# Kernel tuning notes

Hardware: AMD Instinct MI355X
Metric: run time of the kernel (lower is better)

## Reference

```python
import jax, jax.numpy as jnp
import numpy as np

B, CL, H, W, NP = 128, 8, 16, 16, 32   # batch, primary cap length, height, width, n primary capsules
NC, CLO, ITER = 10, 16, 3              # n output capsules, output capsule length, routing iterations


def squash(t):
    # TensorMONK Activations 'squash': squash along axis 2 of a 3D tensor
    ss = jnp.sum(t * t, axis=2, keepdims=True)
    return (ss / (1.0 + ss)) * t / jnp.sqrt(ss)


def setup_inputs() -> dict:
    key = jax.random.key(0)
    k1, k2 = jax.random.split(key)
    tensor = jax.random.normal(k1, (B, CL, H, W, NP), dtype=jnp.float32)
    # nn.Parameter(torch.randn(...).normal_(0.0, 0.1)) -> N(0, 0.1)
    weight = 0.1 * jax.random.normal(k2, (CL * H * W, NP, NC * CLO), dtype=jnp.float32)
    return {"tensor": tensor, "weight": weight}


def reference(tensor, weight):
    b, cl, h, w, n_prim = tensor.shape
    # flatten spatial/length dims, squash along primary-capsule axis (dim 2, faithful to source)
    x = squash(tensor.reshape(b, -1, n_prim))                  # (B, P, N) with P = cl*h*w
    # (B,P,1,N) @ (P,N,K) broadcasted matmul -> (B,P,K)
    u = jnp.einsum('bpn,pnk->bpk', x, weight)
    u = u.reshape(b, cl, h, w, NC, CLO)                        # (B, cl, h, w, NC, CLO)
    bias = jnp.zeros((b, cl, h, w, NC), dtype=tensor.dtype)
    v = None
    for i in range(ITER):  # fixed small iteration count
        c = jax.nn.softmax(bias, axis=4)                       # softmax over output capsules
        s = jnp.einsum('bchwn,bchwnk->bnk', c, u)              # weighted sum over cl,h,w
        v = squash(s)                                          # squash along capsule length (axis 2)
        if i < ITER - 1:
            bias = bias + jnp.einsum('bchwnk,bnk->bchwn', u, v)
    return v
```

## Files before the change

kernel.cpp:

```cpp
#include <hip/hip_runtime.h>

typedef unsigned short u16;
typedef unsigned int u32;
typedef __attribute__((ext_vector_type(8))) short bf16x8;
typedef __attribute__((ext_vector_type(4))) float f32x4;

#define B_   128
#define P_   2048
#define NC_  10
#define F_   160
#define NBLK 512
#define PPB  4
#define NTHR 512

__device__ __forceinline__ u16 f2bf(float f) {
    union { float f; unsigned u; } v; v.f = f;
    unsigned r = v.u + 0x7FFFu + ((v.u >> 16) & 1u);
    return (u16)(r >> 16);
}
__device__ __forceinline__ float bf2f(u16 h) {
    union { unsigned u; float f; } v; v.u = ((unsigned)h) << 16;
    return v.f;
}

__global__ void k_prep(const float* __restrict__ t, const float* __restrict__ w,
                       u16* __restrict__ xb, u16* __restrict__ wb) {
    __shared__ u16 wl[32 * F_];
    const int tid = threadIdx.x;
    if (blockIdx.x < 4096) {
        int g = blockIdx.x * 256 + tid;
        int pair = g >> 2, sub = g & 3;
        int p = pair & 2047, b = pair >> 11;
        const float4* tg = (const float4*)t;
        int fi = pair * 8 + sub * 2;
        float4 va = tg[fi], vb = tg[fi + 1];
        float ss = va.x*va.x + va.y*va.y + va.z*va.z + va.w*va.w
                 + vb.x*vb.x + vb.y*vb.y + vb.z*vb.z + vb.w*vb.w;
        ss += __shfl_xor(ss, 1);
        ss += __shfl_xor(ss, 2);
        float fct = ss / ((1.f + ss) * sqrtf(ss));
        u16 h[8] __attribute__((aligned(16)));
        h[0]=f2bf(va.x*fct); h[1]=f2bf(va.y*fct); h[2]=f2bf(va.z*fct); h[3]=f2bf(va.w*fct);
        h[4]=f2bf(vb.x*fct); h[5]=f2bf(vb.y*fct); h[6]=f2bf(vb.z*fct); h[7]=f2bf(vb.w*fct);
        int sw = sub ^ ((b >> 1) & 3);
        *(uint4*)(xb + (p * 128 + b) * 32 + sw * 8) = *(const uint4*)h;
    } else {
        int p = blockIdx.x - 4096;
        const float4* wp = (const float4*)(w + p * 32 * F_);
        for (int e4 = tid; e4 < 1280; e4 += 256) {
            float4 v = wp[e4];
            u16 h[4] __attribute__((aligned(8)));
            h[0]=f2bf(v.x); h[1]=f2bf(v.y); h[2]=f2bf(v.z); h[3]=f2bf(v.w);
            *(ushort4*)(wl + e4 * 4) = *(const ushort4*)h;
        }
        __syncthreads();
        u16* wo = wb + p * F_ * 32;
        for (int sid = tid; sid < 640; sid += 256) {
            int f = sid >> 2, k0 = (sid & 3) << 3;
            u16 tmp[8] __attribute__((aligned(16)));
#pragma unroll
            for (int j = 0; j < 8; ++j) tmp[j] = wl[(k0 + j) * F_ + f];
            int sw = (sid & 3) ^ ((f >> 1) & 3);
            *(uint4*)(wo + f * 32 + sw * 8) = *(const uint4*)tmp;
        }
    }
}

template<int MODE>
__global__ __launch_bounds__(NTHR, 2) void k_pass(
        const u16* __restrict__ xb, const u16* __restrict__ wb,
        const float* __restrict__ vprev, u16* __restrict__ s_part)
{
    __shared__ u16 xt[2][4096];
    __shared__ u16 wt[2][5120];
    const int tid = threadIdx.x, blk = blockIdx.x;
    const int L = tid & 63, wv = tid >> 6;
    const int q = L >> 4, col = L & 15;
    const int b = wv * 16 + col;
    const int qs = (q ^ ((col >> 1) & 3)) * 8;
    const int p0 = blk * PPB;

    float4 vv[NC_];
    if (MODE != 0) {
#pragma unroll
        for (int n = 0; n < NC_; ++n)
            vv[n] = *(const float4*)(vprev + b * F_ + n * 16 + q * 4);
    }

    f32x4 s_acc[NC_];
#pragma unroll
    for (int n = 0; n < NC_; ++n) s_acc[n] = (f32x4){0.f, 0.f, 0.f, 0.f};

    uint4 r0, r1, r2;
    {
        const uint4* xg = (const uint4*)(xb + (size_t)p0 * 4096);
        const uint4* wg = (const uint4*)(wb + (size_t)p0 * 5120);
        r0 = xg[tid]; r1 = wg[tid];
        if (tid < 128) r2 = wg[tid + 512];
    }

    int cur = 0;
#pragma unroll
    for (int pp = 0; pp < PPB; ++pp) {
        __syncthreads();
        ((uint4*)xt[cur])[tid] = r0;
        ((uint4*)wt[cur])[tid] = r1;
        if (tid < 128) ((uint4*)wt[cur])[512 + tid] = r2;
        if (pp + 1 < PPB) {
            const uint4* xg = (const uint4*)(xb + (size_t)(p0 + pp + 1) * 4096);
            const uint4* wg = (const uint4*)(wb + (size_t)(p0 + pp + 1) * 5120);
            r0 = xg[tid]; r1 = wg[tid];
            if (tid < 128) r2 = wg[tid + 512];
        }
        __syncthreads();

        bf16x8 bfrag = *(const bf16x8*)&xt[cur][b * 32 + qs];
        if (MODE == 0) {
#pragma unroll
            for (int n = 0; n < NC_; ++n) {
                bf16x8 afrag = *(const bf16x8*)&wt[cur][(n * 16 + col) * 32 + qs];
                s_acc[n] = __builtin_amdgcn_mfma_f32_16x16x32_bf16(afrag, bfrag, s_acc[n], 0, 0, 0);
            }
        } else {
            float tt[NC_];
#pragma unroll
            for (int n = 0; n < NC_; ++n) {
                bf16x8 afrag = *(const bf16x8*)&wt[cur][(n * 16 + col) * 32 + qs];
                f32x4 z = {0.f, 0.f, 0.f, 0.f};
                f32x4 acc = __builtin_amdgcn_mfma_f32_16x16x32_bf16(afrag, bfrag, z, 0, 0, 0);
                float tv = acc[0]*vv[n].x + acc[1]*vv[n].y + acc[2]*vv[n].z + acc[3]*vv[n].w;
                tv += __shfl_xor(tv, 16);
                tv += __shfl_xor(tv, 32);
                tt[n] = tv;
            }
            float mx = tt[0];
#pragma unroll
            for (int n = 1; n < NC_; ++n) mx = fmaxf(mx, tt[n]);
            float den = 0.f;
#pragma unroll
            for (int n = 0; n < NC_; ++n) { tt[n] = __expf(tt[n] - mx); den += tt[n]; }
            float inv = 1.f / den;
#pragma unroll
            for (int n = 0; n < NC_; ++n) {
                bf16x8 afrag = *(const bf16x8*)&wt[cur][(n * 16 + col) * 32 + qs];
                f32x4 z = {0.f, 0.f, 0.f, 0.f};
                f32x4 acc = __builtin_amdgcn_mfma_f32_16x16x32_bf16(afrag, bfrag, z, 0, 0, 0);
                float cf = tt[n] * inv;
#pragma unroll
                for (int r = 0; r < 4; ++r) s_acc[n][r] += cf * acc[r];
            }
        }
        cur ^= 1;
    }

    u16* sp = s_part + blk * (B_ * F_);
    const float sc = (MODE == 0) ? 0.1f : 1.f;
#pragma unroll
    for (int n = 0; n < NC_; ++n) {
        u16 h[4] __attribute__((aligned(8)));
#pragma unroll
        for (int r = 0; r < 4; ++r) h[r] = f2bf(s_acc[n][r] * sc);
        *(ushort4*)(sp + n * 2048 + b * 16 + q * 4) = *(const ushort4*)h;
    }
}

template<int ADD>
__global__ void k_red(const u16* __restrict__ s_part,
                      const float* __restrict__ vprev, float* __restrict__ vout) {
    __shared__ float red[32 * 66];
    const int tid = threadIdx.x, blk = blockIdx.x;
    const int pid = tid & 7, part = tid >> 3;
    const uint4* sp4 = (const uint4*)s_part;
    const int base = blk * 8 + pid;
    float a[8];
#pragma unroll
    for (int j = 0; j < 8; ++j) a[j] = 0.f;
    for (int g = part; g < NBLK; g += 32) {
        uint4 uv = sp4[(size_t)g * 2560 + base];
        a[0] += bf2f((u16)(uv.x & 0xffff)); a[1] += bf2f((u16)(uv.x >> 16));
        a[2] += bf2f((u16)(uv.y & 0xffff)); a[3] += bf2f((u16)(uv.y >> 16));
        a[4] += bf2f((u16)(uv.z & 0xffff)); a[5] += bf2f((u16)(uv.z >> 16));
        a[6] += bf2f((u16)(uv.w & 0xffff)); a[7] += bf2f((u16)(uv.w >> 16));
    }
#pragma unroll
    for (int j = 0; j < 8; ++j) red[part * 66 + pid * 8 + j] = a[j];
    __syncthreads();
    if (tid < 32) {
        float s0 = 0.f, s1 = 0.f;
#pragma unroll
        for (int k = 0; k < 32; ++k) {
            s0 += red[k * 66 + tid * 2];
            s1 += red[k * 66 + tid * 2 + 1];
        }
        float sq = s0 * s0 + s1 * s1;
        sq += __shfl_xor(sq, 1);
        sq += __shfl_xor(sq, 2);
        sq += __shfl_xor(sq, 4);
        float fct = sq / ((1.f + sq) * sqrtf(sq));
        const int i = blk * 8 + (tid >> 2);
        const int n = i >> 8, bb = (i & 255) >> 1, hh = i & 1;
        const int f0 = bb * 160 + n * 16 + hh * 8 + 2 * (tid & 3);
        float2 o = make_float2(s0 * fct, s1 * fct);
        if (ADD) {
            float2 pv = *(const float2*)(vprev + f0);
            o.x += pv.x; o.y += pv.y;
        }
        *(float2*)(vout + f0) = o;
    }
}

extern "C" void kernel_launch(void* const* d_in, const int* in_sizes, int n_in,
                              void* d_out, int out_size, void* d_ws, size_t ws_size,
                              hipStream_t stream) {
    const float* tensor = (const float*)d_in[0];
    const float* weight = (const float*)d_in[1];
    float* out = (float*)d_out;
    char* ws = (char*)d_ws;

    u16*   xb     = (u16*)(ws);
    u16*   wb     = (u16*)(ws + 16777216);
    u16*   s_part = (u16*)(ws + 37748736);
    float* v0     = (float*)(ws + 58720256);
    float* vs     = (float*)(ws + 58802176);

    k_prep<<<6144, 256, 0, stream>>>(tensor, weight, xb, wb);

    k_pass<0><<<NBLK, NTHR, 0, stream>>>(xb, wb, nullptr, s_part);
    k_red<0><<<320, 256, 0, stream>>>(s_part, nullptr, v0);
    k_pass<1><<<NBLK, NTHR, 0, stream>>>(xb, wb, v0, s_part);
    k_red<1><<<320, 256, 0, stream>>>(s_part, v0, vs);
    k_pass<2><<<NBLK, NTHR, 0, stream>>>(xb, wb, vs, s_part);
    k_red<0><<<320, 256, 0, stream>>>(s_part, nullptr, out);
}
```

Baseline: 176.4 us.

## Fuse cross-block reduction into pass kernel via atomic ticket, pad prep LDS

New measurement: 250.4 us. 42.0% more time.

```diff
diff --git a/kernel.cpp b/kernel.cpp
--- a/kernel.cpp
+++ b/kernel.cpp
@@ -12,6 +12,9 @@
 #define NBLK 512
 #define PPB  4
 #define NTHR 512
+#define NRED 160
+#define TK0  (NBLK - NRED)
+#define WLS  164
 
 __device__ __forceinline__ u16 f2bf(float f) {
     union { float f; unsigned u; } v; v.f = f;
@@ -24,9 +27,11 @@
 }
 
 __global__ void k_prep(const float* __restrict__ t, const float* __restrict__ w,
-                       u16* __restrict__ xb, u16* __restrict__ wb) {
-    __shared__ u16 wl[32 * F_];
+                       u16* __restrict__ xb, u16* __restrict__ wb,
+                       u32* __restrict__ cnt) {
+    __shared__ u16 wl[32 * WLS];
     const int tid = threadIdx.x;
+    if (blockIdx.x == 0 && tid < 3) cnt[tid] = 0;
     if (blockIdx.x < 4096) {
         int g = blockIdx.x * 256 + tid;
         int pair = g >> 2, sub = g & 3;
@@ -51,7 +56,8 @@
             float4 v = wp[e4];
             u16 h[4] __attribute__((aligned(8)));
             h[0]=f2bf(v.x); h[1]=f2bf(v.y); h[2]=f2bf(v.z); h[3]=f2bf(v.w);
-            *(ushort4*)(wl + e4 * 4) = *(const ushort4*)h;
+            int row = e4 / 40, c4 = e4 % 40;
+            *(ushort4*)(wl + row * WLS + c4 * 4) = *(const ushort4*)h;
         }
         __syncthreads();
         u16* wo = wb + p * F_ * 32;
@@ -59,7 +65,7 @@
             int f = sid >> 2, k0 = (sid & 3) << 3;
             u16 tmp[8] __attribute__((aligned(16)));
 #pragma unroll
-            for (int j = 0; j < 8; ++j) tmp[j] = wl[(k0 + j) * F_ + f];
+            for (int j = 0; j < 8; ++j) tmp[j] = wl[(k0 + j) * WLS + f];
             int sw = (sid & 3) ^ ((f >> 1) & 3);
             *(uint4*)(wo + f * 32 + sw * 8) = *(const uint4*)tmp;
         }
@@ -69,10 +75,13 @@
 template<int MODE>
 __global__ __launch_bounds__(NTHR, 2) void k_pass(
         const u16* __restrict__ xb, const u16* __restrict__ wb,
-        const float* __restrict__ vprev, u16* __restrict__ s_part)
+        const float* __restrict__ vprev, u16* __restrict__ s_part,
+        float* __restrict__ vtgt, u32* __restrict__ cnt)
 {
     __shared__ u16 xt[2][4096];
     __shared__ u16 wt[2][5120];
+    __shared__ float redL[2][32 * 66];
+    __shared__ u32 tkt_s;
     const int tid = threadIdx.x, blk = blockIdx.x;
     const int L = tid & 63, wv = tid >> 6;
     const int q = L >> 4, col = L & 15;
@@ -162,50 +171,68 @@
         for (int r = 0; r < 4; ++r) h[r] = f2bf(s_acc[n][r] * sc);
         *(ushort4*)(sp + n * 2048 + b * 16 + q * 4) = *(const ushort4*)h;
     }
-}
-
-template<int ADD>
-__global__ void k_red(const u16* __restrict__ s_part,
-                      const float* __restrict__ vprev, float* __restrict__ vout) {
-    __shared__ float red[32 * 66];
-    const int tid = threadIdx.x, blk = blockIdx.x;
-    const int pid = tid & 7, part = tid >> 3;
-    const uint4* sp4 = (const uint4*)s_part;
-    const int base = blk * 8 + pid;
-    float a[8];
-#pragma unroll
-    for (int j = 0; j < 8; ++j) a[j] = 0.f;
-    for (int g = part; g < NBLK; g += 32) {
-        uint4 uv = sp4[(size_t)g * 2560 + base];
-        a[0] += bf2f((u16)(uv.x & 0xffff)); a[1] += bf2f((u16)(uv.x >> 16));
-        a[2] += bf2f((u16)(uv.y & 0xffff)); a[3] += bf2f((u16)(uv.y >> 16));
-        a[4] += bf2f((u16)(uv.z & 0xffff)); a[5] += bf2f((u16)(uv.z >> 16));
-        a[6] += bf2f((u16)(uv.w & 0xffff)); a[7] += bf2f((u16)(uv.w >> 16));
-    }
-#pragma unroll
-    for (int j = 0; j < 8; ++j) red[part * 66 + pid * 8 + j] = a[j];
+
     __syncthreads();
-    if (tid < 32) {
-        float s0 = 0.f, s1 = 0.f;
-#pragma unroll
-        for (int k = 0; k < 32; ++k) {
-            s0 += red[k * 66 + tid * 2];
-            s1 += red[k * 66 + tid * 2 + 1];
-        }
-        float sq = s0 * s0 + s1 * s1;
-        sq += __shfl_xor(sq, 1);
-        sq += __shfl_xor(sq, 2);
-        sq += __shfl_xor(sq, 4);
-        float fct = sq / ((1.f + sq) * sqrtf(sq));
-        const int i = blk * 8 + (tid >> 2);
-        const int n = i >> 8, bb = (i & 255) >> 1, hh = i & 1;
-        const int f0 = bb * 160 + n * 16 + hh * 8 + 2 * (tid & 3);
-        float2 o = make_float2(s0 * fct, s1 * fct);
-        if (ADD) {
-            float2 pv = *(const float2*)(vprev + f0);
-            o.x += pv.x; o.y += pv.y;
-        }
-        *(float2*)(vout + f0) = o;
+    if (tid == 0) {
+        __threadfence();
+        tkt_s = atomicAdd(cnt, 1u);
+    }
+    __syncthreads();
+    const u32 tk = tkt_s;
+    if (tk < TK0) return;
+    const int jid2 = (int)tk - TK0;
+    if (jid2 >= NRED) return;
+    if (tid == 0) {
+        int bail = 1 << 26;
+        while (__hip_atomic_load(cnt, __ATOMIC_ACQUIRE,
+                                 __HIP_MEMORY_SCOPE_AGENT) < NBLK && --bail)
+            __builtin_amdgcn_s_sleep(2);
+        __threadfence();
+    }
+    __syncthreads();
+
+    {
+        const int hB = tid >> 8, jtid = tid & 255;
+        const int job = jid2 * 2 + hB;
+        const int pid = jtid & 7, part = jtid >> 3;
+        const uint4* sp4 = (const uint4*)s_part;
+        const int base = job * 8 + pid;
+        float a[8];
+#pragma unroll
+        for (int j = 0; j < 8; ++j) a[j] = 0.f;
+        for (int g = part; g < NBLK; g += 32) {
+            uint4 uv = sp4[(size_t)g * 2560 + base];
+            a[0] += bf2f((u16)(uv.x & 0xffff)); a[1] += bf2f((u16)(uv.x >> 16));
+            a[2] += bf2f((u16)(uv.y & 0xffff)); a[3] += bf2f((u16)(uv.y >> 16));
+            a[4] += bf2f((u16)(uv.z & 0xffff)); a[5] += bf2f((u16)(uv.z >> 16));
+            a[6] += bf2f((u16)(uv.w & 0xffff)); a[7] += bf2f((u16)(uv.w >> 16));
+        }
+        float* rl = redL[hB];
+#pragma unroll
+        for (int j = 0; j < 8; ++j) rl[part * 66 + pid * 8 + j] = a[j];
+        __syncthreads();
+        if (jtid < 32) {
+            float s0 = 0.f, s1 = 0.f;
+#pragma unroll
+            for (int k = 0; k < 32; ++k) {
+                s0 += rl[k * 66 + jtid * 2];
+                s1 += rl[k * 66 + jtid * 2 + 1];
+            }
+            float sq = s0 * s0 + s1 * s1;
+            sq += __shfl_xor(sq, 1);
+            sq += __shfl_xor(sq, 2);
+            sq += __shfl_xor(sq, 4);
+            float fct = sq / ((1.f + sq) * sqrtf(sq));
+            const int i = job * 8 + (jtid >> 2);
+            const int n = i >> 8, bb = (i & 255) >> 1, hh = i & 1;
+            const int f0 = bb * 160 + n * 16 + hh * 8 + 2 * (jtid & 3);
+            float2 o = make_float2(s0 * fct, s1 * fct);
+            if (MODE == 1) {
+                float2 pv = *(const float2*)(vprev + f0);
+                o.x += pv.x; o.y += pv.y;
+            }
+            *(float2*)(vtgt + f0) = o;
+        }
     }
 }
 
@@ -222,13 +249,11 @@
     u16*   s_part = (u16*)(ws + 37748736);
     float* v0     = (float*)(ws + 58720256);
     float* vs     = (float*)(ws + 58802176);
-
-    k_prep<<<6144, 256, 0, stream>>>(tensor, weight, xb, wb);
-
-    k_pass<0><<<NBLK, NTHR, 0, stream>>>(xb, wb, nullptr, s_part);
-    k_red<0><<<320, 256, 0, stream>>>(s_part, nullptr, v0);
-    k_pass<1><<<NBLK, NTHR, 0, stream>>>(xb, wb, v0, s_part);
-    k_red<1><<<320, 256, 0, stream>>>(s_part, v0, vs);
-    k_pass<2><<<NBLK, NTHR, 0, stream>>>(xb, wb, vs, s_part);
-    k_red<0><<<320, 256, 0, stream>>>(s_part, nullptr, out);
-}
+    u32*   cnt    = (u32*)(ws + 58884096);
+
+    k_prep<<<6144, 256, 0, stream>>>(tensor, weight, xb, wb, cnt);
+
+    k_pass<0><<<NBLK, NTHR, 0, stream>>>(xb, wb, nullptr, s_part, v0,  cnt + 0);
+    k_pass<1><<<NBLK, NTHR, 0, stream>>>(xb, wb, v0,      s_part, vs,  cnt + 1);
+    k_pass<2><<<NBLK, NTHR, 0, stream>>>(xb, wb, vs,      s_part, out, cnt + 2);
+}
```
